# Kernel optimization log

Measured on AMD Instinct MI355X. Metric: run time of the kernel, lower is better.

The kernel has to match this reference:

```python
import jax, jax.numpy as jnp
import numpy as np

B, S, D = 2, 2048, 2048
HQ, HKV = 32, 8
HD = D // HQ            # head_dim = 64
G = HQ // HKV           # groups = 4
KV_DIM = HKV * HD       # 512


def setup_inputs() -> dict:
    key = jax.random.key(0)
    ks = jax.random.split(key, 5)
    x = jax.random.normal(ks[0], (B, S, D), dtype=jnp.float32)
    W_q = jax.random.normal(ks[1], (D, D), dtype=jnp.float32) * (1.0 / np.sqrt(D))
    W_k = jax.random.normal(ks[2], (D, KV_DIM), dtype=jnp.float32) * (1.0 / np.sqrt(D))
    W_v = jax.random.normal(ks[3], (D, KV_DIM), dtype=jnp.float32) * (1.0 / np.sqrt(D))
    W_o = jax.random.normal(ks[4], (D, D), dtype=jnp.float32) * (1.0 / np.sqrt(D))
    # causal mask: 1 where attending allowed, 0 elsewhere (masked_fill(mask==0, -inf))
    mask = jnp.tril(jnp.ones((S, S), dtype=jnp.int32))[None, None, :, :]
    return {"x": x, "W_q": W_q, "W_k": W_k, "W_v": W_v, "W_o": W_o, "mask": mask}


def reference(x, W_q, W_k, W_v, W_o, mask):
    scale = np.sqrt(HD).astype(np.float32)
    # projections
    Q = (x @ W_q).reshape(B, S, HQ, HD).transpose(0, 2, 1, 3)    # (B,Hq,S,hd)
    K = (x @ W_k).reshape(B, S, HKV, HD).transpose(0, 2, 1, 3)   # (B,Hkv,S,hd)
    V = (x @ W_v).reshape(B, S, HKV, HD).transpose(0, 2, 1, 3)   # (B,Hkv,S,hd)
    # group Q heads with their shared KV head instead of repeat_interleave
    Qg = Q.reshape(B, HKV, G, S, HD)                             # (B,Hkv,G,S,hd)
    scores = jnp.einsum('bkgsd,bktd->bkgst', Qg, K) / scale      # (B,Hkv,G,S,T)
    m = mask.reshape(1, 1, 1, S, S)
    scores = jnp.where(m == 0, jnp.float32(-jnp.inf), scores)
    attn = jax.nn.softmax(scores, axis=-1)                       # dropout p=0.0
    out_h = jnp.einsum('bkgst,bktd->bkgsd', attn, V)             # (B,Hkv,G,S,hd)
    out_h = out_h.reshape(B, HQ, S, HD).transpose(0, 2, 1, 3).reshape(B, S, D)
    out = out_h @ W_o
    return out, K, V
```

## Files before the change

### kernel.cpp

```cpp
#include <hip/hip_runtime.h>

typedef unsigned short u16;
typedef unsigned int u32;
typedef __attribute__((ext_vector_type(8))) __bf16 bf16x8;
typedef __attribute__((ext_vector_type(8))) u16 u16x8;
typedef __attribute__((ext_vector_type(2))) u32 u32x2;
typedef __attribute__((ext_vector_type(4))) float f32x4;
typedef __attribute__((ext_vector_type(16))) float f32x16;

#define DEVI static __device__ __forceinline__


DEVI u16 f2bf(float f) {
  unsigned u = __float_as_uint(f);
  u += 0x7fff + ((u >> 16) & 1);
  return (u16)(u >> 16);
}

DEVI u32 cvt_pk_bf16(float lo, float hi) {
  u32 r;
  asm("v_cvt_pk_bf16_f32 %0, %1, %2" : "=v"(r) : "v"(lo), "v"(hi));
  return r;
}

DEVI float bperm_f(int srclane, float v) {
  return __int_as_float(__builtin_amdgcn_ds_bpermute(srclane << 2, __float_as_int(v)));
}

DEVI void gll16(const void* g, void* l) {
  __builtin_amdgcn_global_load_lds((const __attribute__((address_space(1))) void*)g,
                                   (__attribute__((address_space(3))) void*)l, 16, 0, 0);
}

DEVI void stage128x32(const u16* g, int ld, u16* lds) {
  int t = threadIdx.x, w = t >> 6, l = t & 63;
#pragma unroll
  for (int r = 0; r < 2; ++r) {
    int c = (w * 2 + r) * 64 + l;
    int row = c >> 2;
    int p = (c & 3) ^ (row & 3);
    gll16(g + (size_t)row * ld + p * 8, (char*)lds + (w * 2 + r) * 1024);
  }
}

DEVI void stage64x64(const u16* g, int ld, u16* lds) {
  int t = threadIdx.x, w = t >> 6, l = t & 63;
#pragma unroll
  for (int r = 0; r < 2; ++r) {
    int c = (w * 2 + r) * 64 + l;
    int row = c >> 3;
    int p = (c & 7) ^ (row & 7);
    gll16(g + (size_t)row * ld + p * 8, (char*)lds + (w * 2 + r) * 1024);
  }
}

DEVI void gemm_tile(const u16* A, int lda, const u16* Bt, int ldb, int K,
                    int m0, int n0, u16* sA, u16* sB, f32x4 acc[4][4]) {
  const int t = threadIdx.x, w = t >> 6, lane = t & 63;
  const int wr = w >> 1, wc = w & 1, g = lane >> 4, r16 = lane & 15;
  int offa[4], offb[4];
#pragma unroll
  for (int m = 0; m < 4; ++m) {
    int row = wr * 64 + m * 16 + r16;
    offa[m] = row * 32 + ((g ^ (row & 3)) << 3);
  }
#pragma unroll
  for (int n = 0; n < 4; ++n) {
    int row = wc * 64 + n * 16 + r16;
    offb[n] = row * 32 + ((g ^ (row & 3)) << 3);
  }
#pragma unroll
  for (int m = 0; m < 4; ++m)
#pragma unroll
    for (int n = 0; n < 4; ++n) acc[m][n] = f32x4{0.f, 0.f, 0.f, 0.f};

  const u16* At = A + (size_t)m0 * lda;
  const u16* Bb = Bt + (size_t)n0 * ldb;
  stage128x32(At, lda, sA);
  stage128x32(Bb, ldb, sB);
  asm volatile("s_waitcnt vmcnt(0)" ::: "memory");
  __syncthreads();
  const int nk = K >> 5;
  int cur = 0;
  for (int kt = 0; kt < nk; ++kt) {
    if (kt + 1 < nk) {
      stage128x32(At + (kt + 1) * 32, lda, sA + (cur ^ 1) * 4096);
      stage128x32(Bb + (kt + 1) * 32, ldb, sB + (cur ^ 1) * 4096);
    }
    bf16x8 av[4], bv[4];
#pragma unroll
    for (int m = 0; m < 4; ++m) av[m] = *(const bf16x8*)(sA + cur * 4096 + offa[m]);
#pragma unroll
    for (int n = 0; n < 4; ++n) bv[n] = *(const bf16x8*)(sB + cur * 4096 + offb[n]);
#pragma unroll
    for (int m = 0; m < 4; ++m)
#pragma unroll
      for (int n = 0; n < 4; ++n)
        acc[m][n] = __builtin_amdgcn_mfma_f32_16x16x32_bf16(av[m], bv[n], acc[m][n], 0, 0, 0);
    asm volatile("s_waitcnt vmcnt(0)" ::: "memory");
    __syncthreads();
    cur ^= 1;
  }
}

__global__ __launch_bounds__(256) void cvt_kernel(const float* __restrict__ src,
                                                  u16* __restrict__ dst) {
  int i = blockIdx.x * 256 + threadIdx.x;
  float4 a = ((const float4*)src)[2 * i];
  float4 b = ((const float4*)src)[2 * i + 1];
  u16x8 o;
  o[0] = f2bf(a.x); o[1] = f2bf(a.y); o[2] = f2bf(a.z); o[3] = f2bf(a.w);
  o[4] = f2bf(b.x); o[5] = f2bf(b.y); o[6] = f2bf(b.z); o[7] = f2bf(b.w);
  ((u16x8*)dst)[i] = o;
}

__global__ __launch_bounds__(256) void transpose_all(
    const float* __restrict__ wq, const float* __restrict__ wk,
    const float* __restrict__ wv, const float* __restrict__ wo,
    u16* __restrict__ wqT, u16* __restrict__ wkT,
    u16* __restrict__ wvT, u16* __restrict__ woT) {
  __shared__ float tle[32][33];
  int bxr = blockIdx.x;
  const float* src; u16* dst; int C, bxl;
  if (bxr < 64)       { src = wq; dst = wqT; C = 2048; bxl = bxr; }
  else if (bxr < 80)  { src = wk; dst = wkT; C = 512;  bxl = bxr - 64; }
  else if (bxr < 96)  { src = wv; dst = wvT; C = 512;  bxl = bxr - 80; }
  else                { src = wo; dst = woT; C = 2048; bxl = bxr - 96; }
  int bx = bxl * 32, by = blockIdx.y * 32;
  int tx = threadIdx.x, ty = threadIdx.y;
#pragma unroll
  for (int i = 0; i < 32; i += 8) tle[ty + i][tx] = src[(size_t)(by + ty + i) * C + bx + tx];
  __syncthreads();
#pragma unroll
  for (int i = 0; i < 32; i += 8)
    dst[(size_t)(bx + ty + i) * 2048 + by + tx] = f2bf(tle[tx][ty + i]);
}

__global__ __launch_bounds__(256) void proj_kernel(
    const u16* __restrict__ x, const u16* __restrict__ wqT, const u16* __restrict__ wkT,
    const u16* __restrict__ wvT, u16* __restrict__ qout, float* __restrict__ koutf,
    u16* __restrict__ kbf, float* __restrict__ voutf, u16* __restrict__ vtout) {
  __shared__ __align__(16) u16 sA[2 * 4096];
  __shared__ __align__(16) u16 sB[2 * 4096];
  const int bid = blockIdx.x;
  int mode, bm, bn;
  const u16* Bt;
  if (bid < 512) { mode = 0; bm = bid >> 4; bn = bid & 15; Bt = wqT; }
  else if (bid < 640) { mode = 1; int i = bid - 512; bm = i >> 2; bn = i & 3; Bt = wkT; }
  else { mode = 2; int i = bid - 640; bm = i >> 2; bn = i & 3; Bt = wvT; }

  f32x4 acc[4][4];
  gemm_tile(x, 2048, Bt, 2048, 2048, bm * 128, bn * 128, sA, sB, acc);

  const int t = threadIdx.x, w = t >> 6, lane = t & 63;
  const int wr = w >> 1, wc = w & 1, g = lane >> 4, r16 = lane & 15;
  const float QSCALE = 0.125f * 1.44269504088896340736f;
#pragma unroll
  for (int m = 0; m < 4; ++m)
#pragma unroll
    for (int n = 0; n < 4; ++n)
#pragma unroll
      for (int j = 0; j < 4; ++j) {
        int row = bm * 128 + wr * 64 + m * 16 + g * 4 + j;
        int col = bn * 128 + wc * 64 + n * 16 + r16;
        float v = acc[m][n][j];
        if (mode == 0) {
          qout[(size_t)row * 2048 + col] = f2bf(v * QSCALE);
        } else {
          int b = row >> 11, s = row & 2047;
          int h = col >> 6, d = col & 63;
          size_t idx = ((size_t)(b * 8 + h) * 2048 + s) * 64 + d;
          if (mode == 1) {
            koutf[idx] = v;
            kbf[idx] = f2bf(v);
          } else {
            voutf[idx] = v;
            vtout[((size_t)(b * 8 + h) * 64 + d) * 2048 + s] = f2bf(v);
          }
        }
      }
}

DEVI void attn_tile32(const u16* sKc, const u16* sVc, u16* sPw,
                      const bf16x8 (&qf)[4], f32x16 (&accO0)[1], f32x16 (&accO1)[1],
                      float &mi, float &li,
                      int wrow0, int kv0, int lane,
                      const int (&offk)[2][4], const int (&offv)[4][2],
                      const int (&offp)[4]) {
  if (kv0 > wrow0 + 31) return;
  const int l5 = lane >> 5, l31 = lane & 31;
  f32x16 st[2];
#pragma unroll
  for (int i = 0; i < 16; ++i) { st[0][i] = 0.f; st[1][i] = 0.f; }
  __builtin_amdgcn_s_setprio(1);
#pragma unroll
  for (int kd = 0; kd < 4; ++kd)
#pragma unroll
    for (int kb = 0; kb < 2; ++kb) {
      bf16x8 kf = *(const bf16x8*)(sKc + offk[kb][kd]);
      st[kb] = __builtin_amdgcn_mfma_f32_32x32x16_bf16(kf, qf[kd], st[kb], 0, 0, 0);
    }
  __builtin_amdgcn_s_setprio(0);
  if (kv0 + 63 > wrow0) {
    int qg = wrow0 + l31;
#pragma unroll
    for (int kb = 0; kb < 2; ++kb)
#pragma unroll
      for (int r = 0; r < 16; ++r) {
        int kvg = kv0 + kb * 32 + (r & 3) + 8 * (r >> 2) + 4 * l5;
        if (kvg > qg) st[kb][r] = -1e30f;
      }
  }
  float pmax = st[0][0];
#pragma unroll
  for (int r = 1; r < 16; ++r) pmax = fmaxf(pmax, st[0][r]);
#pragma unroll
  for (int r = 0; r < 16; ++r) pmax = fmaxf(pmax, st[1][r]);
  pmax = fmaxf(pmax, __shfl_xor(pmax, 32));
  if (!__all(pmax - mi <= 8.0f)) {
    float mn = fmaxf(mi, pmax);
    float scl = exp2f(mi - mn);
    mi = mn; li *= scl;
#pragma unroll
    for (int r = 0; r < 16; ++r) {
      int qp = (r & 3) + 8 * (r >> 2) + 4 * l5;
      float sj = bperm_f(qp, scl);
      accO0[0][r] *= sj;
      accO1[0][r] *= sj;
    }
  }
  float rs = 0.f;
#pragma unroll
  for (int kb = 0; kb < 2; ++kb)
#pragma unroll
    for (int r = 0; r < 16; ++r) { st[kb][r] = exp2f(st[kb][r] - mi); rs += st[kb][r]; }
  rs += __shfl_xor(rs, 32);
  li += rs;
  {
    u16* base = sPw + l31 * 64;
#pragma unroll
    for (int kb = 0; kb < 2; ++kb)
#pragma unroll
      for (int tt = 0; tt < 4; ++tt) {
        u32 lo = cvt_pk_bf16(st[kb][4 * tt + 0], st[kb][4 * tt + 1]);
        u32 hi = cvt_pk_bf16(st[kb][4 * tt + 2], st[kb][4 * tt + 3]);
        int chunk = kb * 4 + tt;
        u32x2 w2 = {lo, hi};
        *(u32x2*)(base + ((chunk ^ (l31 & 7)) << 3) + l5 * 4) = w2;
      }
  }
  asm volatile("s_waitcnt lgkmcnt(0)" ::: "memory");
  __builtin_amdgcn_s_setprio(1);
#pragma unroll
  for (int ks = 0; ks < 4; ++ks) {
    bf16x8 pa = *(const bf16x8*)(sPw + offp[ks]);
    bf16x8 v0 = *(const bf16x8*)(sVc + offv[ks][0]);
    bf16x8 v1 = *(const bf16x8*)(sVc + offv[ks][1]);
    accO0[0] = __builtin_amdgcn_mfma_f32_32x32x16_bf16(pa, v0, accO0[0], 0, 0, 0);
    accO1[0] = __builtin_amdgcn_mfma_f32_32x32x16_bf16(pa, v1, accO1[0], 0, 0, 0);
  }
  __builtin_amdgcn_s_setprio(0);
}

__global__ __launch_bounds__(256) void attn_kernel(
    const u16* __restrict__ Q, const u16* __restrict__ Kp,
    const u16* __restrict__ Vt, u16* __restrict__ Oh) {
  __shared__ __align__(16) u16 sK[2][4096];
  __shared__ __align__(16) u16 sV[2][4096];
  __shared__ __align__(16) u16 sP[4][2048];
  const int bid = blockIdx.x;
  const int xcd = bid & 7, rank = bid >> 3;
  const int qb = 15 - (rank >> 3);
  const int sub = rank & 7;
  const int bhkv = xcd * 2 + (sub >> 2);
  const int b = bhkv >> 3, hkv = bhkv & 7;
  const int h = hkv * 4 + (sub & 3);
  const int t = threadIdx.x, w = t >> 6, lane = t & 63;
  const int l5 = lane >> 5, l31 = lane & 31;
  const int wrow0 = qb * 128 + w * 32;

  int offk[2][4], offv[4][2], offp[4];
#pragma unroll
  for (int kb = 0; kb < 2; ++kb) {
    int row = kb * 32 + l31;
#pragma unroll
    for (int kd = 0; kd < 4; ++kd)
      offk[kb][kd] = row * 64 + (((kd * 2 + l5) ^ (row & 7)) << 3);
  }
#pragma unroll
  for (int ks = 0; ks < 4; ++ks) {
    offp[ks] = l31 * 64 + (((ks * 2 + l5) ^ (l31 & 7)) << 3);
#pragma unroll
    for (int nd = 0; nd < 2; ++nd) {
      int rd = nd * 32 + l31;
      offv[ks][nd] = rd * 64 + (((ks * 2 + l5) ^ (rd & 7)) << 3);
    }
  }

  const u16* Qb = Q + (size_t)b * 2048 * 2048 + h * 64 + l5 * 8;
  bf16x8 qf[4];
#pragma unroll
  for (int kd = 0; kd < 4; ++kd)
    qf[kd] = *(const bf16x8*)(Qb + (size_t)(wrow0 + l31) * 2048 + kd * 16);

  const u16* Kh = Kp + (size_t)(b * 8 + hkv) * 2048 * 64;
  const u16* Vh = Vt + (size_t)(b * 8 + hkv) * 64 * 2048;

  f32x16 ao0[1], ao1[1];
#pragma unroll
  for (int i = 0; i < 16; ++i) { ao0[0][i] = 0.f; ao1[0][i] = 0.f; }
  float mi = -1e30f, li = 0.f;

  const int nt = 2 * (qb + 1);
  int cur = 0;
  stage64x64(Kh, 64, sK[0]);
  stage64x64(Vh, 2048, sV[0]);
  for (int it = 0; it < nt; ++it) {
    asm volatile("s_waitcnt vmcnt(0)" ::: "memory");
    __syncthreads();
    if (it + 1 < nt) {
      stage64x64(Kh + (size_t)(it + 1) * 64 * 64, 64, sK[cur ^ 1]);
      stage64x64(Vh + (it + 1) * 64, 2048, sV[cur ^ 1]);
    }
    const int kv0 = it * 64;
    attn_tile32(sK[cur], sV[cur], sP[w], qf, ao0, ao1, mi, li, wrow0, kv0, lane, offk, offv, offp);
    cur ^= 1;
  }
  float rl = 1.0f / li;
#pragma unroll
  for (int r = 0; r < 16; ++r) {
    int qp = (r & 3) + 8 * (r >> 2) + 4 * l5;
    float f = bperm_f(qp, rl);
    size_t row = (size_t)b * 2048 + wrow0 + qp;
    int col = h * 64 + l31;
    Oh[row * 2048 + col]      = f2bf(ao0[0][r] * f);
    Oh[row * 2048 + col + 32] = f2bf(ao1[0][r] * f);
  }
}

__global__ __launch_bounds__(256) void outproj_kernel(const u16* __restrict__ A,
                                                      const u16* __restrict__ WoT,
                                                      float* __restrict__ out) {
  __shared__ __align__(16) u16 sA[2 * 4096];
  __shared__ __align__(16) u16 sB[2 * 4096];
  const int bm = blockIdx.x >> 4, bn = blockIdx.x & 15;
  f32x4 acc[4][4];
  gemm_tile(A, 2048, WoT, 2048, 2048, bm * 128, bn * 128, sA, sB, acc);
  const int t = threadIdx.x, w = t >> 6, lane = t & 63;
  const int wr = w >> 1, wc = w & 1, g = lane >> 4, r16 = lane & 15;
#pragma unroll
  for (int m = 0; m < 4; ++m)
#pragma unroll
    for (int n = 0; n < 4; ++n)
#pragma unroll
      for (int j = 0; j < 4; ++j) {
        int row = bm * 128 + wr * 64 + m * 16 + g * 4 + j;
        int col = bn * 128 + wc * 64 + n * 16 + r16;
        out[(size_t)row * 2048 + col] = acc[m][n][j];
      }
}

extern "C" void kernel_launch(void* const* d_in, const int* in_sizes, int n_in,
                              void* d_out, int out_size, void* d_ws, size_t ws_size,
                              hipStream_t stream) {
  const float* x  = (const float*)d_in[0];
  const float* wq = (const float*)d_in[1];
  const float* wk = (const float*)d_in[2];
  const float* wv = (const float*)d_in[3];
  const float* wo = (const float*)d_in[4];

  const size_t NEED_BYTES = 2ull * (8388608 + 4194304 + 1048576 + 1048576 + 4194304);
  if (ws_size < NEED_BYTES) return;

  float* outf  = (float*)d_out;
  float* koutf = outf + (size_t)8388608;
  float* voutf = koutf + (size_t)2097152;

  u16* Qs  = (u16*)d_out;
  u16* Vt  = Qs + (size_t)8388608;
  u16* Kbf = Vt + (size_t)2097152;

  u16* ws   = (u16*)d_ws;
  u16* xbf  = ws;
  u16* Oh   = ws;
  u16* wqT  = ws  + (size_t)8388608;
  u16* wkT  = wqT + (size_t)4194304;
  u16* wvT  = wkT + (size_t)1048576;
  u16* woT  = wvT + (size_t)1048576;

  cvt_kernel<<<4096, 256, 0, stream>>>(x, xbf);
  transpose_all<<<dim3(160, 64), dim3(32, 8), 0, stream>>>(wq, wk, wv, wo, wqT, wkT, wvT, woT);

  proj_kernel<<<768, 256, 0, stream>>>(xbf, wqT, wkT, wvT, Qs, koutf, Kbf, voutf, Vt);
  attn_kernel<<<1024, 256, 0, stream>>>(Qs, Kbf, Vt, Oh);
  outproj_kernel<<<512, 256, 0, stream>>>(Oh, woT, outf);
}
```

Measured before the change: 233.8 us.

## Split long causal attention rows across two blocks with a combine pass

Query blocks 8-15, which have the longest causal KV ranges, are now split into two halves over the KV range, each handled by its own workgroup, so there are 1536 blocks instead of 1024. Each half writes an unnormalized partial output along with its row max and sum, and a new combine kernel merges the halves with log-sum-exp weights. This targets load imbalance and tail latency from long causal rows. In exchange it adds an extra launch and extra global traffic, stores partials in bf16, and drops the XCD-aware block mapping, which may reduce L2 reuse of K/V.

New measurement: 239.8 us. 1.03x slower.

```diff
diff --git a/kernel.cpp b/kernel.cpp
--- a/kernel.cpp
+++ b/kernel.cpp
@@ -264,17 +264,25 @@
 
 __global__ __launch_bounds__(256) void attn_kernel(
     const u16* __restrict__ Q, const u16* __restrict__ Kp,
-    const u16* __restrict__ Vt, u16* __restrict__ Oh) {
+    const u16* __restrict__ Vt, u16* __restrict__ Oh,
+    u16* __restrict__ pO, float* __restrict__ pm1, float* __restrict__ pl1,
+    float* __restrict__ pm2, float* __restrict__ pl2) {
   __shared__ __align__(16) u16 sK[2][4096];
   __shared__ __align__(16) u16 sV[2][4096];
   __shared__ __align__(16) u16 sP[4][2048];
   const int bid = blockIdx.x;
-  const int xcd = bid & 7, rank = bid >> 3;
-  const int qb = 15 - (rank >> 3);
-  const int sub = rank & 7;
-  const int bhkv = xcd * 2 + (sub >> 2);
-  const int b = bhkv >> 3, hkv = bhkv & 7;
-  const int h = hkv * 4 + (sub & 3);
+  int qb, bh, it0, it1, mode2;
+  if (bid < 512) {
+    int idx = bid; qb = 8 + (idx >> 6); bh = idx & 63;
+    it0 = 0; it1 = qb + 1; mode2 = 1;
+  } else if (bid < 1024) {
+    int idx = bid - 512; qb = 8 + (idx >> 6); bh = idx & 63;
+    it0 = qb + 1; it1 = 2 * (qb + 1); mode2 = 2;
+  } else {
+    int idx = bid - 1024; qb = 7 - (idx >> 6); bh = idx & 63;
+    it0 = 0; it1 = 2 * (qb + 1); mode2 = 0;
+  }
+  const int b = bh >> 5, h = bh & 31, hkv = h >> 2;
   const int t = threadIdx.x, w = t >> 6, lane = t & 63;
   const int l5 = lane >> 5, l31 = lane & 31;
   const int wrow0 = qb * 128 + w * 32;
@@ -311,14 +319,13 @@
   for (int i = 0; i < 16; ++i) { ao0[0][i] = 0.f; ao1[0][i] = 0.f; }
   float mi = -1e30f, li = 0.f;
 
-  const int nt = 2 * (qb + 1);
   int cur = 0;
-  stage64x64(Kh, 64, sK[0]);
-  stage64x64(Vh, 2048, sV[0]);
-  for (int it = 0; it < nt; ++it) {
+  stage64x64(Kh + (size_t)it0 * 64 * 64, 64, sK[0]);
+  stage64x64(Vh + it0 * 64, 2048, sV[0]);
+  for (int it = it0; it < it1; ++it) {
     asm volatile("s_waitcnt vmcnt(0)" ::: "memory");
     __syncthreads();
-    if (it + 1 < nt) {
+    if (it + 1 < it1) {
       stage64x64(Kh + (size_t)(it + 1) * 64 * 64, 64, sK[cur ^ 1]);
       stage64x64(Vh + (it + 1) * 64, 2048, sV[cur ^ 1]);
     }
@@ -326,15 +333,68 @@
     attn_tile32(sK[cur], sV[cur], sP[w], qf, ao0, ao1, mi, li, wrow0, kv0, lane, offk, offv, offp);
     cur ^= 1;
   }
-  float rl = 1.0f / li;
-#pragma unroll
-  for (int r = 0; r < 16; ++r) {
-    int qp = (r & 3) + 8 * (r >> 2) + 4 * l5;
-    float f = bperm_f(qp, rl);
-    size_t row = (size_t)b * 2048 + wrow0 + qp;
-    int col = h * 64 + l31;
-    Oh[row * 2048 + col]      = f2bf(ao0[0][r] * f);
-    Oh[row * 2048 + col + 32] = f2bf(ao1[0][r] * f);
+
+  if (mode2 == 0) {
+    float rl = 1.0f / li;
+#pragma unroll
+    for (int r = 0; r < 16; ++r) {
+      int qp = (r & 3) + 8 * (r >> 2) + 4 * l5;
+      float f = bperm_f(qp, rl);
+      size_t row = (size_t)b * 2048 + wrow0 + qp;
+      int col = h * 64 + l31;
+      Oh[row * 2048 + col]      = f2bf(ao0[0][r] * f);
+      Oh[row * 2048 + col + 32] = f2bf(ao1[0][r] * f);
+    }
+  } else {
+    const int p = (qb - 8) * 64 + bh;
+#pragma unroll
+    for (int r = 0; r < 16; ++r) {
+      int qp = (r & 3) + 8 * (r >> 2) + 4 * l5;
+      if (mode2 == 1) {
+        u16* po = pO + (size_t)p * 8192 + (w * 32 + qp) * 64 + l31;
+        po[0]  = f2bf(ao0[0][r]);
+        po[32] = f2bf(ao1[0][r]);
+      } else {
+        size_t row = (size_t)b * 2048 + wrow0 + qp;
+        int col = h * 64 + l31;
+        Oh[row * 2048 + col]      = f2bf(ao0[0][r]);
+        Oh[row * 2048 + col + 32] = f2bf(ao1[0][r]);
+      }
+    }
+    if (l5 == 0) {
+      int ridx = p * 128 + w * 32 + l31;
+      if (mode2 == 1) { pm1[ridx] = mi; pl1[ridx] = li; }
+      else            { pm2[ridx] = mi; pl2[ridx] = li; }
+    }
+  }
+}
+
+__global__ __launch_bounds__(256) void combine_kernel(
+    const u16* __restrict__ pO, const float* __restrict__ pm1, const float* __restrict__ pl1,
+    const float* __restrict__ pm2, const float* __restrict__ pl2, u16* __restrict__ Oh) {
+  const int p = blockIdx.x;
+  const int qb = 8 + (p >> 6), bh = p & 63, b = bh >> 5, h = bh & 31;
+  const int t = threadIdx.x, row = t >> 1, half = t & 1;
+  const int ridx = p * 128 + row;
+  float m1 = pm1[ridx], l1 = pl1[ridx], m2 = pm2[ridx], l2 = pl2[ridx];
+  float m = fmaxf(m1, m2);
+  float w1 = exp2f(m1 - m), w2 = exp2f(m2 - m);
+  float dn = 1.0f / (l1 * w1 + l2 * w2);
+  w1 *= dn; w2 *= dn;
+  const u16* po = pO + (size_t)p * 8192 + row * 64 + half * 32;
+  u16* oh = Oh + ((size_t)b * 2048 + qb * 128 + row) * 2048 + h * 64 + half * 32;
+#pragma unroll
+  for (int v = 0; v < 4; ++v) {
+    u16x8 a = *(const u16x8*)(po + v * 8);
+    u16x8 c = *(const u16x8*)(oh + v * 8);
+    u16x8 o;
+#pragma unroll
+    for (int i = 0; i < 8; ++i) {
+      float o1 = __uint_as_float(((u32)a[i]) << 16);
+      float o2 = __uint_as_float(((u32)c[i]) << 16);
+      o[i] = f2bf(o1 * w1 + o2 * w2);
+    }
+    *(u16x8*)(oh + v * 8) = o;
   }
 }
 
@@ -388,10 +448,17 @@
   u16* wvT  = wkT + (size_t)1048576;
   u16* woT  = wvT + (size_t)1048576;
 
+  u16*   pO  = wqT;
+  float* pm1 = (float*)wkT;
+  float* pl1 = pm1 + 65536;
+  float* pm2 = pl1 + 65536;
+  float* pl2 = pm2 + 65536;
+
   cvt_kernel<<<4096, 256, 0, stream>>>(x, xbf);
   transpose_all<<<dim3(160, 64), dim3(32, 8), 0, stream>>>(wq, wk, wv, wo, wqT, wkT, wvT, woT);
 
   proj_kernel<<<768, 256, 0, stream>>>(xbf, wqT, wkT, wvT, Qs, koutf, Kbf, voutf, Vt);
-  attn_kernel<<<1024, 256, 0, stream>>>(Qs, Kbf, Vt, Oh);
+  attn_kernel<<<1536, 256, 0, stream>>>(Qs, Kbf, Vt, Oh, pO, pm1, pl1, pm2, pl2);
+  combine_kernel<<<512, 256, 0, stream>>>(pO, pm1, pl1, pm2, pl2, Oh);
   outproj_kernel<<<512, 256, 0, stream>>>(Oh, woT, outf);
 }
```
